# Kernel optimization log

Hardware: AMD Instinct MI355X
Metric: run time of the kernel (lower is better)

The kernel has to match this reference:

```python
import jax, jax.numpy as jnp
import numpy as np

B, C, HF, WF = 64, 512, 28, 28
HID = 512
NUM_CLS = 30
LOC_REG = 8
MAX_LEN = 500  # loop runs MAX_LEN + 1 = 501 steps


def setup_inputs() -> dict:
    key = jax.random.key(0)
    ks = jax.random.split(key, 12)
    sc = 0.02
    rn = lambda k, shape: jax.random.normal(k, shape, jnp.float32) * sc
    z = lambda shape: jnp.zeros(shape, jnp.float32)
    return {
        "fea": jax.random.normal(ks[0], (B, C, HF, WF), jnp.float32),
        # AttentionGRUCell params
        "i2h_w": rn(ks[1], (HID, C)),            # Linear(C, H, bias=False)
        "h2h_w": rn(ks[2], (HID, HID)),
        "h2h_b": z((HID,)),
        "score_w": rn(ks[3], (1, HID)),          # Linear(H, 1, bias=False)
        "gru_w_ih": rn(ks[4], (3 * HID, C + NUM_CLS)),
        "gru_w_hh": rn(ks[5], (3 * HID, HID)),
        "gru_b_ih": z((3 * HID,)),
        "gru_b_hh": z((3 * HID,)),
        # structure_generator: Linear(H,H) -> Linear(H, NUM_CLS) (no activation)
        "sg1_w": rn(ks[6], (HID, HID)), "sg1_b": z((HID,)),
        "sg2_w": rn(ks[7], (NUM_CLS, HID)), "sg2_b": z((NUM_CLS,)),
        # loc_generator: Linear(H,H) -> Linear(H, LOC_REG) -> Sigmoid
        "lg1_w": rn(ks[8], (HID, HID)), "lg1_b": z((HID,)),
        "lg2_w": rn(ks[9], (LOC_REG, HID)), "lg2_b": z((LOC_REG,)),
    }


def reference(fea, i2h_w, h2h_w, h2h_b, score_w, gru_w_ih, gru_w_hh,
              gru_b_ih, gru_b_hh, sg1_w, sg1_b, sg2_w, sg2_b,
              lg1_w, lg1_b, lg2_w, lg2_b):
    b = fea.shape[0]
    feat = fea.reshape(b, fea.shape[1], -1).transpose(0, 2, 1)      # [B, T, C]
    # i2h(batch_H) is step-invariant: hoist it out of the decode loop
    feat_proj = jnp.einsum('btc,hc->bth', feat, i2h_w)              # [B, T, H]
    sv = score_w[0]                                                  # [H]

    def gru_cell(x, h):
        gi = x @ gru_w_ih.T + gru_b_ih
        gh = h @ gru_w_hh.T + gru_b_hh
        i_r, i_z, i_n = jnp.split(gi, 3, axis=-1)
        h_r, h_z, h_n = jnp.split(gh, 3, axis=-1)
        r = jax.nn.sigmoid(i_r + h_r)
        z = jax.nn.sigmoid(i_z + h_z)
        n = jnp.tanh(i_n + r * h_n)
        return (1.0 - z) * n + z * h

    def step(carry, _):
        hidden, pre_chars = carry
        onehot = jax.nn.one_hot(pre_chars, NUM_CLS, dtype=feat.dtype)
        hproj = hidden @ h2h_w.T + h2h_b                             # [B, H]
        e = jnp.einsum('bth,h->bt', jnp.tanh(feat_proj + hproj[:, None, :]), sv)
        alpha = jax.nn.softmax(e, axis=1)                            # [B, T]
        context = jnp.einsum('bt,btc->bc', alpha, feat)              # [B, C]
        x = jnp.concatenate([context, onehot], axis=1)               # [B, C+NUM_CLS]
        new_hidden = gru_cell(x, hidden)
        structure_step = (new_hidden @ sg1_w.T + sg1_b) @ sg2_w.T + sg2_b
        loc_step = jax.nn.sigmoid((new_hidden @ lg1_w.T + lg1_b) @ lg2_w.T + lg2_b)
        new_chars = jnp.argmax(structure_step, axis=1)               # greedy decode
        return (new_hidden, new_chars), (structure_step, loc_step)

    hidden0 = jnp.zeros((b, HID), feat.dtype)
    chars0 = jnp.zeros((b,), jnp.int32)
    _, (structs, locs) = jax.lax.scan(step, (hidden0, chars0), None, length=MAX_LEN + 1)
    structure_probs = jax.nn.softmax(structs.transpose(1, 0, 2), axis=-1)  # eval-mode softmax
    loc_preds = locs.transpose(1, 0, 2)
    return structure_probs, loc_preds
```

## Files before the change

### kernel.cpp

```cpp
#include <hip/hip_runtime.h>
#include <hip/hip_bf16.h>


#define NB 64
#define TT 784
#define CC 512
#define HH 512
#define NCLS 30
#define LREG 8
#define STEPS 501
#define GRID_MAIN 256
#define THR_MAIN 1024

typedef float floatx2 __attribute__((ext_vector_type(2)));

struct SlaP {
  __hip_bfloat16* feat16;
  unsigned char* scr8;
  float* hid2;
  float* hproj;
  float* h1sg;
  float* h1lg;
  float* ctx2;
  float* wsum;
  int*   chars;
  unsigned* bar;
  const float *score_w, *w_ih, *w_hh, *b_ih, *b_hh;
  const float *h2h_w, *h2h_b, *sg1_w, *sg1_b, *sg2_w, *sg2_b;
  const float *lg1_w, *lg1_b, *lg2_w, *lg2_b;
  float *out_probs, *out_loc;
};

__device__ __forceinline__ float lo16(unsigned v){ return __uint_as_float(v << 16); }
__device__ __forceinline__ float hi16(unsigned v){ return __uint_as_float(v & 0xffff0000u); }

__device__ __forceinline__ float cld(const float* p){
  return __hip_atomic_load(p, __ATOMIC_RELAXED, __HIP_MEMORY_SCOPE_AGENT);
}
__device__ __forceinline__ void cst(float* p, float v){
  __hip_atomic_store(p, v, __ATOMIC_RELAXED, __HIP_MEMORY_SCOPE_AGENT);
}
__device__ __forceinline__ int cldi(const int* p){
  return __hip_atomic_load(p, __ATOMIC_RELAXED, __HIP_MEMORY_SCOPE_AGENT);
}
__device__ __forceinline__ void csti(int* p, int v){
  __hip_atomic_store(p, v, __ATOMIC_RELAXED, __HIP_MEMORY_SCOPE_AGENT);
}
__device__ __forceinline__ float2 cld2(const float* p){
  unsigned long long v = __hip_atomic_load((const unsigned long long*)p,
                          __ATOMIC_RELAXED, __HIP_MEMORY_SCOPE_AGENT);
  union { unsigned long long u; float2 f; } c; c.u = v; return c.f;
}
__device__ __forceinline__ void cst2(float* p, float a, float b){
  union { unsigned long long u; float2 f; } c; c.f = make_float2(a, b);
  __hip_atomic_store((unsigned long long*)p, c.u,
                     __ATOMIC_RELAXED, __HIP_MEMORY_SCOPE_AGENT);
}

__device__ __forceinline__ float tanh_fast(float x){
  float ex = __expf(2.f * x);
  return 1.f - 2.f * __builtin_amdgcn_rcpf(ex + 1.f);
}
__device__ __forceinline__ float sigmoid_fast(float x){
  return __builtin_amdgcn_rcpf(1.f + __expf(-x));
}
__device__ __forceinline__ float warp_sum(float v){
  #pragma unroll
  for (int m = 32; m > 0; m >>= 1) v += __shfl_xor(v, m, 64);
  return v;
}
__device__ __forceinline__ float warp_max(float v){
  #pragma unroll
  for (int m = 32; m > 0; m >>= 1) v = fmaxf(v, __shfl_xor(v, m, 64));
  return v;
}
__device__ __forceinline__ int warp_min_i(int v){
  #pragma unroll
  for (int m = 32; m > 0; m >>= 1) v = min(v, __shfl_xor(v, m, 64));
  return v;
}

__device__ __forceinline__ void gbar(unsigned* bar, unsigned target){
  __syncthreads();
  if (threadIdx.x == 0){
    unsigned* c8 = bar + 8 + (blockIdx.x & 7) * 32;
    unsigned p = __hip_atomic_fetch_add(c8, 1u, __ATOMIC_RELAXED, __HIP_MEMORY_SCOPE_AGENT);
    if (p == 32u * target - 1u){
      unsigned pm = __hip_atomic_fetch_add(bar, 1u, __ATOMIC_RELAXED, __HIP_MEMORY_SCOPE_AGENT);
      if (pm == 8u * target - 1u)
        __hip_atomic_store(bar + 64, target, __ATOMIC_RELAXED, __HIP_MEMORY_SCOPE_AGENT);
    }
    while (__hip_atomic_load(bar + 64, __ATOMIC_RELAXED, __HIP_MEMORY_SCOPE_AGENT) < target)
      __builtin_amdgcn_s_sleep(1);
  }
  __syncthreads();
}


__global__ void k_init(SlaP p){
  int idx = blockIdx.x * blockDim.x + threadIdx.x;
  if (idx < 32768){ p.hid2[idx] = 0.f; p.ctx2[idx] = 0.f; }
  if (idx < 64*512) p.hproj[idx] = p.h2h_b[idx & 511];
  if (idx < 64){ p.wsum[idx] = 0.f; p.chars[idx] = 0; }
  if (idx < 512) p.bar[idx] = 0u;
}

__global__ void k_transpose(const float* __restrict__ fea, __hip_bfloat16* __restrict__ feat16){
  __shared__ float tile[64][65];
  const int b = blockIdx.z, t0 = blockIdx.x * 64, c0 = blockIdx.y * 64;
  #pragma unroll
  for (int r = 0; r < 16; ++r){
    int idx = threadIdx.x + 256*r;
    int ci = idx >> 6, tj = idx & 63;
    float v = 0.f;
    if (t0 + tj < TT) v = fea[((size_t)b*CC + (c0+ci))*TT + t0 + tj];
    tile[ci][tj] = v;
  }
  __syncthreads();
  #pragma unroll
  for (int r = 0; r < 16; ++r){
    int idx = threadIdx.x + 256*r;
    int tj = idx >> 6, ci = idx & 63;
    if (t0 + tj < TT)
      feat16[((size_t)b*TT + t0 + tj)*CC + c0 + ci] = __float2bfloat16(tile[ci][tj]);
  }
}

__global__ void k_fpgemm(const float* __restrict__ fea, const float* __restrict__ i2h,
                         unsigned char* __restrict__ scr8){
  const int b = blockIdx.z, t0 = blockIdx.x * 64, h0 = blockIdx.y * 64;
  const int tx = threadIdx.x & 15, ty = threadIdx.x >> 4;
  const int tb = t0 + tx*4, hb = h0 + ty*4;
  const int ts = (tb < TT) ? tb : 0;
  const float* A = fea + (size_t)b*CC*TT;
  float acc[4][4];
  #pragma unroll
  for (int j = 0; j < 4; ++j)
    #pragma unroll
    for (int i2 = 0; i2 < 4; ++i2) acc[j][i2] = 0.f;
  for (int k = 0; k < CC; ++k){
    const float4 a4 = *(const float4*)&A[(size_t)k*TT + ts];
    float bv0 = i2h[(size_t)(hb+0)*CC + k];
    float bv1 = i2h[(size_t)(hb+1)*CC + k];
    float bv2 = i2h[(size_t)(hb+2)*CC + k];
    float bv3 = i2h[(size_t)(hb+3)*CC + k];
    acc[0][0] += bv0*a4.x; acc[0][1] += bv0*a4.y; acc[0][2] += bv0*a4.z; acc[0][3] += bv0*a4.w;
    acc[1][0] += bv1*a4.x; acc[1][1] += bv1*a4.y; acc[1][2] += bv1*a4.z; acc[1][3] += bv1*a4.w;
    acc[2][0] += bv2*a4.x; acc[2][1] += bv2*a4.y; acc[2][2] += bv2*a4.z; acc[2][3] += bv2*a4.w;
    acc[3][0] += bv3*a4.x; acc[3][1] += bv3*a4.y; acc[3][2] += bv3*a4.z; acc[3][3] += bv3*a4.w;
  }
  if (tb < TT){
    #pragma unroll
    for (int i2 = 0; i2 < 4; ++i2){
      int pk = __builtin_amdgcn_cvt_pk_fp8_f32(acc[0][i2], acc[1][i2], 0, false);
      pk = __builtin_amdgcn_cvt_pk_fp8_f32(acc[2][i2], acc[3][i2], pk, true);
      *(int*)&scr8[((size_t)b*TT + tb + i2)*512 + hb] = pk;
    }
  }
}


__global__ void __launch_bounds__(THR_MAIN, 4) sla_main(SlaP p){
  const int tid  = threadIdx.x;
  const int lane = tid & 63;
  const int wv   = tid >> 6;
  const int blk  = blockIdx.x;
  __shared__ float sm[12352];
  __shared__ uint4 lsc4[6272];
  unsigned char* lsc = (unsigned char*)lsc4;
  float* smF = sm + 12288;

  const int ab = blk >> 2;
  const int aslice = blk & 3;
  float svr[8];
  #pragma unroll
  for (int k = 0; k < 8; ++k) svr[k] = p.score_w[lane*8 + k];

  const int cnt = (wv < 4) ? 13 : 12;
  const int r0r = wv*12 + ((wv < 4) ? wv : 4);

  unsigned bid = 0;

  for (int i = 0; i <= STEPS; ++i){
    if (i > 0 && blk < NB){
      const int fb = blk;
      for (int task = wv; task < 38; task += 16){
        const float* wrow; const float* src; float bias;
        if (task < 30){ wrow = p.sg2_w + task*512; bias = p.sg2_b[task]; src = p.h1sg + fb*512; }
        else          { wrow = p.lg2_w + (task-30)*512; bias = p.lg2_b[task-30]; src = p.h1lg + fb*512; }
        float s = 0.f;
        #pragma unroll
        for (int kq = 0; kq < 4; ++kq){
          const float2 wv2 = *(const float2*)&wrow[lane*2 + 128*kq];
          const float2 sv2 = cld2(&src[lane*2 + 128*kq]);
          s += wv2.x*sv2.x + wv2.y*sv2.y;
        }
        s = warp_sum(s);
        if (task < 30){ if (lane == 0) smF[task] = s + bias; }
        else if (lane == 0)
          p.out_loc[(size_t)fb*(STEPS*LREG) + (size_t)(i-1)*LREG + (task-30)] = sigmoid_fast(s + bias);
      }
    }
    __syncthreads();
    if (i > 0 && blk < NB && wv == 0){
      float sv_ = (lane < 30) ? smF[lane] : -3.4e38f;
      float m = warp_max(sv_);
      float e = (lane < 30) ? __expf(sv_ - m) : 0.f;
      float ssum = warp_sum(e);
      if (lane < 30)
        p.out_probs[(size_t)blk*(STEPS*NCLS) + (size_t)(i-1)*NCLS + lane] = e / ssum;
      int cand = (lane < 30 && sv_ == m) ? lane : 1000;
      cand = warp_min_i(cand);
      if (lane == 0) csti(&p.chars[blk], cand);
    }
    if (i == STEPS) break;
    if (i == 0){
      const uint4* g = (const uint4*)(p.scr8 + ((size_t)ab*TT + aslice*196)*512);
      for (int idx = tid; idx < 6272; idx += THR_MAIN) lsc4[idx] = g[idx];
      __syncthreads();
    }
    {
      float hpr[8];
      #pragma unroll
      for (int k = 0; k < 4; ++k){
        float2 h2 = cld2(&p.hproj[ab*512 + lane*8 + 2*k]);
        hpr[2*k] = h2.x; hpr[2*k+1] = h2.y;
      }
      float e[13];
      #pragma unroll
      for (int r = 0; r < 13; ++r){
        if (r < cnt){
          const uint2 rd = *(const uint2*)&lsc[(r0r + r)*512 + lane*8];
          const floatx2 p01 = __builtin_amdgcn_cvt_pk_f32_fp8(rd.x, false);
          const floatx2 p23 = __builtin_amdgcn_cvt_pk_f32_fp8(rd.x, true);
          const floatx2 p45 = __builtin_amdgcn_cvt_pk_f32_fp8(rd.y, false);
          const floatx2 p67 = __builtin_amdgcn_cvt_pk_f32_fp8(rd.y, true);
          float s = 0.f;
          s += tanh_fast(p01.x + hpr[0]) * svr[0];
          s += tanh_fast(p01.y + hpr[1]) * svr[1];
          s += tanh_fast(p23.x + hpr[2]) * svr[2];
          s += tanh_fast(p23.y + hpr[3]) * svr[3];
          s += tanh_fast(p45.x + hpr[4]) * svr[4];
          s += tanh_fast(p45.y + hpr[5]) * svr[5];
          s += tanh_fast(p67.x + hpr[6]) * svr[6];
          s += tanh_fast(p67.y + hpr[7]) * svr[7];
          e[r] = s;
        } else e[r] = 0.f;
      }
      #pragma unroll
      for (int m = 32; m > 0; m >>= 1){
        #pragma unroll
        for (int r = 0; r < 13; ++r) e[r] += __shfl_xor(e[r], m, 64);
      }
      float w[13];
      float wsr = 0.f;
      #pragma unroll
      for (int r = 0; r < 13; ++r){
        if (r < cnt){ w[r] = __expf(e[r]); wsr += w[r]; }
        else w[r] = 0.f;
      }
      const int fwd = ((i & 1) == 0);
      const unsigned short* ftB = (const unsigned short*)p.feat16 +
                                  ((size_t)ab*TT + aslice*196)*512 + lane*8;
      float acc[8] = {0,0,0,0,0,0,0,0};
      uint4 buf[4];
      #pragma unroll
      for (int j = 0; j < 4; ++j){
        const int row = fwd ? (r0r + j) : (r0r + cnt - 1 - j);
        buf[j] = *(const uint4*)(ftB + (size_t)row*512);
      }
      #pragma unroll
      for (int r = 0; r < 13; ++r){
        if (r < cnt){
          const uint4 ct = buf[r & 3];
          if (r + 4 < cnt){
            const int row = fwd ? (r0r + r + 4) : (r0r + cnt - 1 - (r + 4));
            buf[r & 3] = *(const uint4*)(ftB + (size_t)row*512);
          }
          const int ri = fwd ? r : (cnt - 1 - r);
          const float wg = w[ri];
          acc[0] += wg*lo16(ct.x); acc[1] += wg*hi16(ct.x);
          acc[2] += wg*lo16(ct.y); acc[3] += wg*hi16(ct.y);
          acc[4] += wg*lo16(ct.z); acc[5] += wg*hi16(ct.z);
          acc[6] += wg*lo16(ct.w); acc[7] += wg*hi16(ct.w);
        }
      }
      if (wv < 8){
        #pragma unroll
        for (int k = 0; k < 8; ++k) sm[wv*512 + lane*8 + k] = acc[k];
      }
      if (lane == 0) smF[32 + wv] = wsr;
      __syncthreads();
      if (wv >= 8){
        #pragma unroll
        for (int k = 0; k < 8; ++k) sm[(wv-8)*512 + lane*8 + k] += acc[k];
      }
      __syncthreads();
      if (tid < 512){
        float s = 0.f;
        #pragma unroll
        for (int r = 0; r < 8; ++r) s += sm[r*512 + tid];
        unsafeAtomicAdd(&p.ctx2[(tid >> 1)*128 + ab*2 + (tid & 1)], s);
      } else if (tid == 512){
        float s = 0.f;
        #pragma unroll
        for (int r = 0; r < 16; ++r) s += smF[32 + r];
        unsafeAtomicAdd(&p.wsum[ab], s);
      }
    }
    gbar(p.bar, ++bid);
    if (blk < 128){
      const int j0 = blk * 4;
      const float* hidC = p.hid2 + (i & 1)*(512*64);
      float accI[4][3], accH[4][3];
      #pragma unroll
      for (int jj = 0; jj < 4; ++jj)
        #pragma unroll
        for (int g = 0; g < 3; ++g){ accI[jj][g] = 0.f; accH[jj][g] = 0.f; }
      const int kb = wv * 32;
      for (int kk = 0; kk < 32; kk += 4){
        const int k = kb + kk;
        const float2 x01 = cld2(&p.ctx2[(k >> 1)*128 + lane*2]);
        const float2 x23 = cld2(&p.ctx2[(k >> 1)*128 + 128 + lane*2]);
        const float2 h01 = cld2(&hidC[(k >> 1)*128 + lane*2]);
        const float2 h23 = cld2(&hidC[(k >> 1)*128 + 128 + lane*2]);
        #pragma unroll
        for (int jj = 0; jj < 4; ++jj)
          #pragma unroll
          for (int g = 0; g < 3; ++g){
            const int row = g*512 + j0 + jj;
            const float4 wi = *(const float4*)&p.w_ih[(size_t)row*542 + k];
            const float4 wh = *(const float4*)&p.w_hh[(size_t)row*512 + k];
            accI[jj][g] += wi.x*x01.x + wi.y*x01.y + wi.z*x23.x + wi.w*x23.y;
            accH[jj][g] += wh.x*h01.x + wh.y*h01.y + wh.z*h23.x + wh.w*h23.y;
          }
      }
      const int slot = wv & 7;
      if (wv < 8){
        #pragma unroll
        for (int jj = 0; jj < 4; ++jj)
          #pragma unroll
          for (int g = 0; g < 3; ++g){
            sm[((slot*24) + jj*6 + g    )*64 + lane] = accI[jj][g];
            sm[((slot*24) + jj*6 + 3 + g)*64 + lane] = accH[jj][g];
          }
      }
      __syncthreads();
      if (wv >= 8){
        #pragma unroll
        for (int jj = 0; jj < 4; ++jj)
          #pragma unroll
          for (int g = 0; g < 3; ++g){
            sm[((slot*24) + jj*6 + g    )*64 + lane] += accI[jj][g];
            sm[((slot*24) + jj*6 + 3 + g)*64 + lane] += accH[jj][g];
          }
      }
      __syncthreads();
      if (tid < 128){
        const int pp = tid >> 6;
        const int b = tid & 63;
        const float inv = 1.f / cld(&p.wsum[b]);
        const int ch = cldi(&p.chars[b]);
        const float2 ho = cld2(&hidC[((j0 >> 1) + pp)*128 + b*2]);
        float nh[2];
        #pragma unroll
        for (int q = 0; q < 2; ++q){
          const int jj = pp*2 + q;
          float gi[3], gh[3];
          #pragma unroll
          for (int g = 0; g < 3; ++g){
            float giS = 0.f, ghS = 0.f;
            #pragma unroll
            for (int sl = 0; sl < 8; ++sl){
              giS += sm[((sl*24) + jj*6 + g    )*64 + b];
              ghS += sm[((sl*24) + jj*6 + 3 + g)*64 + b];
            }
            const int row = g*512 + j0 + jj;
            gi[g] = giS*inv + p.w_ih[(size_t)row*542 + 512 + ch] + p.b_ih[row];
            gh[g] = ghS + p.b_hh[row];
          }
          float r_ = sigmoid_fast(gi[0] + gh[0]);
          float z_ = sigmoid_fast(gi[1] + gh[1]);
          float n_ = tanh_fast(gi[2] + r_*gh[2]);
          float hold = (q == 0) ? ho.x : ho.y;
          nh[q] = (1.f - z_)*n_ + z_*hold;
        }
        cst2(&p.hid2[((i+1) & 1)*(512*64) + ((j0 >> 1) + pp)*128 + b*2], nh[0], nh[1]);
      }
    } else {
      __syncthreads(); __syncthreads();
    }
    gbar(p.bar, ++bid);
    if (blk < 128){
      const int r0 = blk * 12;
      const float* hidN = p.hid2 + ((i+1) & 1)*(512*64);
      const float* rowp[12];
      #pragma unroll
      for (int r = 0; r < 12; ++r){
        const int rg = r0 + r, head = rg >> 9, j = rg & 511;
        const float* base = (head == 0) ? p.h2h_w : (head == 1) ? p.sg1_w : p.lg1_w;
        rowp[r] = base + (size_t)j*512;
      }
      float acc[12];
      #pragma unroll
      for (int r = 0; r < 12; ++r) acc[r] = 0.f;
      const int kb = wv * 32;
      for (int kk = 0; kk < 32; kk += 4){
        const int k = kb + kk;
        const float2 h01 = cld2(&hidN[(k >> 1)*128 + lane*2]);
        const float2 h23 = cld2(&hidN[(k >> 1)*128 + 128 + lane*2]);
        #pragma unroll
        for (int r = 0; r < 12; ++r){
          const float4 w4 = *(const float4*)&rowp[r][k];
          acc[r] += w4.x*h01.x + w4.y*h01.y + w4.z*h23.x + w4.w*h23.y;
        }
      }
      const int slot = wv & 7;
      if (wv < 8){
        #pragma unroll
        for (int r = 0; r < 12; ++r) sm[((slot*12) + r)*64 + lane] = acc[r];
      }
      __syncthreads();
      if (wv >= 8){
        #pragma unroll
        for (int r = 0; r < 12; ++r) sm[((slot*12) + r)*64 + lane] += acc[r];
      }
      __syncthreads();
      if (tid < 384){
        const int q = tid >> 6, b = tid & 63;
        float s0 = 0.f, s1 = 0.f;
        #pragma unroll
        for (int sl = 0; sl < 8; ++sl){
          s0 += sm[((sl*12) + 2*q    )*64 + b];
          s1 += sm[((sl*12) + 2*q + 1)*64 + b];
        }
        const int rg = r0 + 2*q, head = rg >> 9, j = rg & 511;
        const float* bb = (head == 0) ? p.h2h_b : (head == 1) ? p.sg1_b : p.lg1_b;
        float* dst = (head == 0) ? p.hproj : (head == 1) ? p.h1sg : p.h1lg;
        cst2(&dst[b*512 + j], s0 + bb[j], s1 + bb[j+1]);
      }
    } else {
      const int bz = blk - 128;
      if (tid < 256) cst(&p.ctx2[bz*256 + tid], 0.f);
      if (bz == 127 && tid < 64) cst(&p.wsum[tid], 0.f);
      __syncthreads(); __syncthreads();
    }
    gbar(p.bar, ++bid);
  }
}

extern "C" void kernel_launch(void* const* d_in, const int* in_sizes, int n_in,
                              void* d_out, int out_size, void* d_ws, size_t ws_size,
                              hipStream_t stream){
  (void)in_sizes; (void)n_in; (void)out_size; (void)ws_size;
  char* w = (char*)d_ws;
  size_t off = 0;
  auto carve = [&](size_t bytes) -> char* {
    char* r = w + off; off += (bytes + 255) & ~(size_t)255; return r;
  };
  SlaP p;
  p.feat16 = (__hip_bfloat16*)carve((size_t)NB*TT*CC*2);
  p.scr8   = (unsigned char*)carve((size_t)NB*TT*HH);
  p.hid2   = (float*)carve((size_t)2*512*64*4);
  p.hproj  = (float*)carve((size_t)64*512*4);
  p.h1sg   = (float*)carve((size_t)64*512*4);
  p.h1lg   = (float*)carve((size_t)64*512*4);
  p.ctx2   = (float*)carve((size_t)512*64*4);
  p.wsum   = (float*)carve(64*4);
  p.chars  = (int*)carve(64*4);
  p.bar    = (unsigned*)carve(2048);

  p.score_w = (const float*)d_in[4];
  p.w_ih  = (const float*)d_in[5];  p.w_hh  = (const float*)d_in[6];
  p.b_ih  = (const float*)d_in[7];  p.b_hh  = (const float*)d_in[8];
  p.h2h_w = (const float*)d_in[2];  p.h2h_b = (const float*)d_in[3];
  p.sg1_w = (const float*)d_in[9];  p.sg1_b = (const float*)d_in[10];
  p.sg2_w = (const float*)d_in[11]; p.sg2_b = (const float*)d_in[12];
  p.lg1_w = (const float*)d_in[13]; p.lg1_b = (const float*)d_in[14];
  p.lg2_w = (const float*)d_in[15]; p.lg2_b = (const float*)d_in[16];
  p.out_probs = (float*)d_out;
  p.out_loc   = p.out_probs + (size_t)NB*STEPS*NCLS;

  const float* fea = (const float*)d_in[0];
  const float* i2h = (const float*)d_in[1];

  k_init<<<128, 256, 0, stream>>>(p);
  k_transpose<<<dim3(13, 8, 64), 256, 0, stream>>>(fea, p.feat16);
  k_fpgemm<<<dim3(13, 8, 64), 256, 0, stream>>>(fea, i2h, p.scr8);
  sla_main<<<GRID_MAIN, THR_MAIN, 0, stream>>>(p);
}
```

Before: 42.34 ms.

## Store transposed features as fp8 and prefetch GEMV activations into registers

```diff
diff --git a/kernel.cpp b/kernel.cpp
--- a/kernel.cpp
+++ b/kernel.cpp
@@ -15,7 +15,7 @@
 typedef float floatx2 __attribute__((ext_vector_type(2)));
 
 struct SlaP {
-  __hip_bfloat16* feat16;
+  unsigned char* feat8;
   unsigned char* scr8;
   float* hid2;
   float* hproj;
@@ -31,9 +31,6 @@
   float *out_probs, *out_loc;
 };
 
-__device__ __forceinline__ float lo16(unsigned v){ return __uint_as_float(v << 16); }
-__device__ __forceinline__ float hi16(unsigned v){ return __uint_as_float(v & 0xffff0000u); }
-
 __device__ __forceinline__ float cld(const float* p){
   return __hip_atomic_load(p, __ATOMIC_RELAXED, __HIP_MEMORY_SCOPE_AGENT);
 }
@@ -105,7 +102,7 @@
   if (idx < 512) p.bar[idx] = 0u;
 }
 
-__global__ void k_transpose(const float* __restrict__ fea, __hip_bfloat16* __restrict__ feat16){
+__global__ void k_feat8(const float* __restrict__ fea, unsigned char* __restrict__ feat8){
   __shared__ float tile[64][65];
   const int b = blockIdx.z, t0 = blockIdx.x * 64, c0 = blockIdx.y * 64;
   #pragma unroll
@@ -118,11 +115,16 @@
   }
   __syncthreads();
   #pragma unroll
-  for (int r = 0; r < 16; ++r){
+  for (int r = 0; r < 4; ++r){
     int idx = threadIdx.x + 256*r;
-    int tj = idx >> 6, ci = idx & 63;
-    if (t0 + tj < TT)
-      feat16[((size_t)b*TT + t0 + tj)*CC + c0 + ci] = __float2bfloat16(tile[ci][tj]);
+    int t = idx >> 4, cg = idx & 15;
+    if (t0 + t < TT){
+      float a = tile[cg*4+0][t], b2 = tile[cg*4+1][t];
+      float c = tile[cg*4+2][t], d = tile[cg*4+3][t];
+      int pk = __builtin_amdgcn_cvt_pk_fp8_f32(a, b2, 0, false);
+      pk = __builtin_amdgcn_cvt_pk_fp8_f32(c, d, pk, true);
+      *(int*)&feat8[((size_t)b*TT + t0 + t)*512 + c0 + cg*4] = pk;
+    }
   }
 }
 
@@ -220,6 +222,12 @@
       __syncthreads();
     }
     {
+      const unsigned char* ftB = p.feat8 + ((size_t)ab*TT + aslice*196)*512 + lane*8;
+      uint2 fv[13];
+      #pragma unroll
+      for (int r = 0; r < 13; ++r)
+        if (r < cnt) fv[r] = *(const uint2*)(ftB + (size_t)(r0r + r)*512);
+
       float hpr[8];
       #pragma unroll
       for (int k = 0; k < 4; ++k){
@@ -259,30 +267,19 @@
         if (r < cnt){ w[r] = __expf(e[r]); wsr += w[r]; }
         else w[r] = 0.f;
       }
-      const int fwd = ((i & 1) == 0);
-      const unsigned short* ftB = (const unsigned short*)p.feat16 +
-                                  ((size_t)ab*TT + aslice*196)*512 + lane*8;
       float acc[8] = {0,0,0,0,0,0,0,0};
-      uint4 buf[4];
-      #pragma unroll
-      for (int j = 0; j < 4; ++j){
-        const int row = fwd ? (r0r + j) : (r0r + cnt - 1 - j);
-        buf[j] = *(const uint4*)(ftB + (size_t)row*512);
-      }
       #pragma unroll
       for (int r = 0; r < 13; ++r){
         if (r < cnt){
-          const uint4 ct = buf[r & 3];
-          if (r + 4 < cnt){
-            const int row = fwd ? (r0r + r + 4) : (r0r + cnt - 1 - (r + 4));
-            buf[r & 3] = *(const uint4*)(ftB + (size_t)row*512);
-          }
-          const int ri = fwd ? r : (cnt - 1 - r);
-          const float wg = w[ri];
-          acc[0] += wg*lo16(ct.x); acc[1] += wg*hi16(ct.x);
-          acc[2] += wg*lo16(ct.y); acc[3] += wg*hi16(ct.y);
-          acc[4] += wg*lo16(ct.z); acc[5] += wg*hi16(ct.z);
-          acc[6] += wg*lo16(ct.w); acc[7] += wg*hi16(ct.w);
+          const floatx2 f01 = __builtin_amdgcn_cvt_pk_f32_fp8(fv[r].x, false);
+          const floatx2 f23 = __builtin_amdgcn_cvt_pk_f32_fp8(fv[r].x, true);
+          const floatx2 f45 = __builtin_amdgcn_cvt_pk_f32_fp8(fv[r].y, false);
+          const floatx2 f67 = __builtin_amdgcn_cvt_pk_f32_fp8(fv[r].y, true);
+          const float wg = w[r];
+          acc[0] += wg*f01.x; acc[1] += wg*f01.y;
+          acc[2] += wg*f23.x; acc[3] += wg*f23.y;
+          acc[4] += wg*f45.x; acc[5] += wg*f45.y;
+          acc[6] += wg*f67.x; acc[7] += wg*f67.y;
         }
       }
       if (wv < 8){
@@ -312,28 +309,34 @@
     if (blk < 128){
       const int j0 = blk * 4;
       const float* hidC = p.hid2 + (i & 1)*(512*64);
+      const int kp0 = wv * 16;
       float accI[4][3], accH[4][3];
       #pragma unroll
       for (int jj = 0; jj < 4; ++jj)
         #pragma unroll
         for (int g = 0; g < 3; ++g){ accI[jj][g] = 0.f; accH[jj][g] = 0.f; }
-      const int kb = wv * 32;
-      for (int kk = 0; kk < 32; kk += 4){
-        const int k = kb + kk;
-        const float2 x01 = cld2(&p.ctx2[(k >> 1)*128 + lane*2]);
-        const float2 x23 = cld2(&p.ctx2[(k >> 1)*128 + 128 + lane*2]);
-        const float2 h01 = cld2(&hidC[(k >> 1)*128 + lane*2]);
-        const float2 h23 = cld2(&hidC[(k >> 1)*128 + 128 + lane*2]);
-        #pragma unroll
-        for (int jj = 0; jj < 4; ++jj)
+      #pragma unroll
+      for (int h = 0; h < 2; ++h){
+        float2 xv[8], hv[8];
+        #pragma unroll
+        for (int t = 0; t < 8; ++t){
+          xv[t] = cld2(&p.ctx2[(kp0 + h*8 + t)*128 + lane*2]);
+          hv[t] = cld2(&hidC[(kp0 + h*8 + t)*128 + lane*2]);
+        }
+        #pragma unroll
+        for (int q = 0; q < 4; ++q){
+          const int k = wv*32 + h*16 + q*4;
           #pragma unroll
-          for (int g = 0; g < 3; ++g){
-            const int row = g*512 + j0 + jj;
-            const float4 wi = *(const float4*)&p.w_ih[(size_t)row*542 + k];
-            const float4 wh = *(const float4*)&p.w_hh[(size_t)row*512 + k];
-            accI[jj][g] += wi.x*x01.x + wi.y*x01.y + wi.z*x23.x + wi.w*x23.y;
-            accH[jj][g] += wh.x*h01.x + wh.y*h01.y + wh.z*h23.x + wh.w*h23.y;
-          }
+          for (int jj = 0; jj < 4; ++jj)
+            #pragma unroll
+            for (int g = 0; g < 3; ++g){
+              const int row = g*512 + j0 + jj;
+              const float4 wi = *(const float4*)&p.w_ih[(size_t)row*542 + k];
+              const float4 wh = *(const float4*)&p.w_hh[(size_t)row*512 + k];
+              accI[jj][g] += wi.x*xv[2*q].x + wi.y*xv[2*q].y + wi.z*xv[2*q+1].x + wi.w*xv[2*q+1].y;
+              accH[jj][g] += wh.x*hv[2*q].x + wh.y*hv[2*q].y + wh.z*hv[2*q+1].x + wh.w*hv[2*q+1].y;
+            }
+        }
       }
       const int slot = wv & 7;
       if (wv < 8){
@@ -401,18 +404,20 @@
         const float* base = (head == 0) ? p.h2h_w : (head == 1) ? p.sg1_w : p.lg1_w;
         rowp[r] = base + (size_t)j*512;
       }
+      float2 hv[16];
+      #pragma unroll
+      for (int t = 0; t < 16; ++t)
+        hv[t] = cld2(&hidN[(wv*16 + t)*128 + lane*2]);
       float acc[12];
       #pragma unroll
       for (int r = 0; r < 12; ++r) acc[r] = 0.f;
-      const int kb = wv * 32;
-      for (int kk = 0; kk < 32; kk += 4){
-        const int k = kb + kk;
-        const float2 h01 = cld2(&hidN[(k >> 1)*128 + lane*2]);
-        const float2 h23 = cld2(&hidN[(k >> 1)*128 + 128 + lane*2]);
+      #pragma unroll
+      for (int q = 0; q < 8; ++q){
+        const int k = wv*32 + q*4;
         #pragma unroll
         for (int r = 0; r < 12; ++r){
           const float4 w4 = *(const float4*)&rowp[r][k];
-          acc[r] += w4.x*h01.x + w4.y*h01.y + w4.z*h23.x + w4.w*h23.y;
+          acc[r] += w4.x*hv[2*q].x + w4.y*hv[2*q].y + w4.z*hv[2*q+1].x + w4.w*hv[2*q+1].y;
         }
       }
       const int slot = wv & 7;
@@ -459,7 +464,7 @@
     char* r = w + off; off += (bytes + 255) & ~(size_t)255; return r;
   };
   SlaP p;
-  p.feat16 = (__hip_bfloat16*)carve((size_t)NB*TT*CC*2);
+  p.feat8  = (unsigned char*)carve((size_t)NB*TT*CC);
   p.scr8   = (unsigned char*)carve((size_t)NB*TT*HH);
   p.hid2   = (float*)carve((size_t)2*512*64*4);
   p.hproj  = (float*)carve((size_t)64*512*4);
@@ -485,7 +490,7 @@
   const float* i2h = (const float*)d_in[1];
 
   k_init<<<128, 256, 0, stream>>>(p);
-  k_transpose<<<dim3(13, 8, 64), 256, 0, stream>>>(fea, p.feat16);
+  k_feat8<<<dim3(13, 8, 64), 256, 0, stream>>>(fea, p.feat8);
   k_fpgemm<<<dim3(13, 8, 64), 256, 0, stream>>>(fea, i2h, p.scr8);
   sla_main<<<GRID_MAIN, THR_MAIN, 0, stream>>>(p);
 }
```

Measured after the change: 77.47 ms. 1.83x slower.
